# Kernel tuning notes

Measured on AMD Instinct MI355X. Metric: run time of the kernel, lower is better.

## Reference

```python
import jax, jax.numpy as jnp
import numpy as np

N = 50000          # nodes (multiple of p+e=8)
E = 400000         # edges (avg degree 8)
H, C = 4, 128      # heads, per-head channels
IN = 5             # input node feature dim
HID = 512          # mlp hidden dim
P, EV = 4, 4       # pursuers / evaders per graph
NEG_SLOPE = 0.2    # GATConv leaky_relu slope

# static team index: nodes with idx % (P+EV) < P  (team='pursuer')
_idx = np.arange(N)
TEAM_IDX = jnp.asarray(_idx[_idx % (P + EV) < P])  # [N/2]


def setup_inputs() -> dict:
    key = jax.random.key(0)
    ks = jax.random.split(key, 16)
    s = 0.1
    return {
        "x": jax.random.normal(ks[0], (N, IN), jnp.float32),
        "edge_index": jax.random.randint(ks[1], (2, E), 0, N, jnp.int64),
        "edge_attr": jax.random.normal(ks[2], (E, 2), jnp.float32),
        # GATConv params
        "W": jax.random.normal(ks[3], (H * C, IN), jnp.float32) * s,
        "att_src": jax.random.normal(ks[4], (H, C), jnp.float32) * s,
        "att_dst": jax.random.normal(ks[5], (H, C), jnp.float32) * s,
        "bias": jnp.zeros((H * C,), jnp.float32),
        # MLP head params
        "W1": jax.random.normal(ks[6], (HID, H * C), jnp.float32) * s,
        "b1": jnp.zeros((HID,), jnp.float32),
        "W2": jax.random.normal(ks[7], (HID, HID), jnp.float32) * s,
        "b2": jnp.zeros((HID,), jnp.float32),
        "W3": jax.random.normal(ks[8], (2, HID), jnp.float32) * s,
        "b3": jnp.zeros((2,), jnp.float32),
    }


def _gat_max(x, src, dst, W, att_src, att_dst, bias):
    # linear transform: [N, H, C]
    h = (x @ W.T).reshape(N, H, C)
    a_src = jnp.einsum("nhc,hc->nh", h, att_src)  # [N, H]
    a_dst = jnp.einsum("nhc,hc->nh", h, att_dst)  # [N, H]
    # per-edge attention logits, leaky relu
    alpha = jax.nn.leaky_relu(a_src[src] + a_dst[dst], NEG_SLOPE)  # [Et, H]
    # segment softmax over incoming edges of each dst node
    amax = jax.ops.segment_max(alpha, dst, num_segments=N)  # [N, H]
    ex = jnp.exp(alpha - amax[dst])
    den = jax.ops.segment_sum(ex, dst, num_segments=N)      # [N, H]
    attn = ex / den[dst]                                     # [Et, H]
    # alpha-weighted messages, scatter-MAX aggregation (aggr='max')
    msg = h[src] * attn[:, :, None]                          # [Et, H, C]
    out = jax.ops.segment_max(msg, dst, num_segments=N)     # [N, H, C]
    return out.reshape(N, H * C) + bias


def reference(x, edge_index, edge_attr, W, att_src, att_dst, bias,
              W1, b1, W2, b2, W3, b3):
    # PyG GATConv default add_self_loops=True; edge_attr ignored (edge_dim=None)
    loops = jnp.arange(N, dtype=edge_index.dtype)
    src = jnp.concatenate([edge_index[0], loops])
    dst = jnp.concatenate([edge_index[1], loops])
    emb = _gat_max(x, src, dst, W, att_src, att_dst, bias)  # [N, 512]
    h = emb[TEAM_IDX]                                        # [N/2, 512]
    h = jax.nn.relu(h @ W1.T + b1)
    h = jax.nn.relu(h @ W2.T + b2)
    return jnp.tanh(h @ W3.T + b3)                           # [N/2, 2]
```

## Files before the change

kernel.cpp:

```cpp
#include <hip/hip_runtime.h>
#include <hip/hip_bf16.h>
#include <math.h>

#define N_NODES 50000
#define N_EDGES 400000
#define HEADS   4
#define HC      512
#define IN_DIM  5
#define M_SEL   25000
#define NEG_SLOPE 0.2f

typedef __attribute__((ext_vector_type(8))) short bf16x8;
typedef __attribute__((ext_vector_type(4))) float f32x4;

__device__ inline unsigned short f2bf(float f) {
    union { float f; unsigned u; } v; v.f = f;
    unsigned r = v.u + 0x7FFF + ((v.u >> 16) & 1);
    return (unsigned short)(r >> 16);
}
__device__ inline float bf2f(unsigned short b) {
    union { unsigned u; float f; } v; v.u = ((unsigned)b) << 16;
    return v.f;
}

#define GLOAD_LDS16(g, l)                                                  \
    __builtin_amdgcn_global_load_lds(                                      \
        (const __attribute__((address_space(1))) unsigned int*)(g),        \
        (__attribute__((address_space(3))) unsigned int*)(l), 16, 0, 0)

__global__ void k_init(const float* __restrict__ W1, const float* __restrict__ W2,
                       unsigned short* __restrict__ W1b, unsigned short* __restrict__ W2b,
                       float* __restrict__ part, int* __restrict__ deg) {
    int i = blockIdx.x * 256 + threadIdx.x;
    const float* src = (i < 65536) ? W1 : W2;
    unsigned short* dst = (i < 65536) ? W1b : W2b;
    int j = i & 65535;
    float4 v = ((const float4*)src)[j];
    ushort4 o;
    o.x = f2bf(v.x); o.y = f2bf(v.y); o.z = f2bf(v.z); o.w = f2bf(v.w);
    ((ushort4*)dst)[j] = o;
    if (i < 2 * M_SEL) part[i] = 0.f;
    if (i < N_NODES) deg[i] = 1;
}

#define TR_NPW 8
#define TR_BLKS 1563

__global__ __launch_bounds__(256) void k_transform_hist(
        const float* __restrict__ x, const float* __restrict__ W,
        const float* __restrict__ att_src, const float* __restrict__ att_dst,
        unsigned short* __restrict__ h, float* __restrict__ a_src,
        float* __restrict__ a_dst, const int* __restrict__ ei,
        int* __restrict__ deg) {
    if (blockIdx.x >= TR_BLKS) {
        int e = (blockIdx.x - TR_BLKS) * 256 + threadIdx.x;
        if (e < N_EDGES) atomicAdd(&deg[ei[N_EDGES + e]], 1);
        return;
    }
    int wave = threadIdx.x >> 6, lane = threadIdx.x & 63;
    int c0 = lane * 8;

    float wreg[40];
    const float4* wp = (const float4*)(W + c0 * IN_DIM);
#pragma unroll
    for (int i = 0; i < 10; i++) ((float4*)wreg)[i] = wp[i];
    float sas[8], sad[8];
    *(float4*)&sas[0] = *(const float4*)(att_src + c0);
    *(float4*)&sas[4] = *(const float4*)(att_src + c0 + 4);
    *(float4*)&sad[0] = *(const float4*)(att_dst + c0);
    *(float4*)&sad[4] = *(const float4*)(att_dst + c0 + 4);

    int n0 = (blockIdx.x * 4 + wave) * TR_NPW;
#pragma unroll
    for (int t = 0; t < TR_NPW; t++) {
        int n = n0 + t;
        if (n >= N_NODES) return;
        float xv[IN_DIM];
#pragma unroll
        for (int i = 0; i < IN_DIM; i++) xv[i] = x[n * IN_DIM + i];

        float ps = 0.f, pd = 0.f;
        bf16x8 hv8;
#pragma unroll
        for (int j = 0; j < 8; j++) {
            float acc = 0.f;
#pragma unroll
            for (int i = 0; i < IN_DIM; i++) acc += xv[i] * wreg[j * IN_DIM + i];
            hv8[j] = (short)f2bf(acc);
            ps += acc * sas[j];
            pd += acc * sad[j];
        }
        *(bf16x8*)(h + (size_t)n * HC + c0) = hv8;

#pragma unroll
        for (int off = 8; off >= 1; off >>= 1) {
            ps += __shfl_xor(ps, off);
            pd += __shfl_xor(pd, off);
        }
        if ((lane & 15) == 0) {
            int head = lane >> 4;
            a_src[n * HEADS + head] = ps;
            a_dst[n * HEADS + head] = pd;
        }
    }
}

#define NSCAN_BLK 196

__global__ void k_scan1(const int* __restrict__ deg, int* __restrict__ excl,
                        int* __restrict__ bsum) {
    __shared__ int s[256];
    int i = blockIdx.x * 256 + threadIdx.x;
    int v = (i < N_NODES) ? deg[i] : 0;
    s[threadIdx.x] = v;
    __syncthreads();
    for (int off = 1; off < 256; off <<= 1) {
        int t = (threadIdx.x >= off) ? s[threadIdx.x - off] : 0;
        __syncthreads();
        s[threadIdx.x] += t;
        __syncthreads();
    }
    if (i < N_NODES) excl[i] = s[threadIdx.x] - v;
    if (threadIdx.x == 255) bsum[blockIdx.x] = s[255];
}

__global__ void k_scan3fill(const int* __restrict__ excl, const int* __restrict__ bsum,
                            int* __restrict__ offs, int* __restrict__ curs,
                            int* __restrict__ csr) {
    __shared__ int part[256];
    int tid = threadIdx.x;
    part[tid] = (tid < NSCAN_BLK) ? bsum[tid] : 0;
    __syncthreads();
    for (int off = 1; off < 256; off <<= 1) {
        int t = (tid >= off) ? part[tid - off] : 0;
        __syncthreads();
        part[tid] += t;
        __syncthreads();
    }
    int blockoff = (blockIdx.x == 0) ? 0 : part[blockIdx.x - 1];
    int i = blockIdx.x * 256 + tid;
    if (i < N_NODES) {
        int o = excl[i] + blockoff;
        offs[i] = o;
        csr[o] = i;
        curs[i] = o + 1;
    }
}

__global__ void k_fill_edges(const int* __restrict__ ei, int* __restrict__ cursor,
                             int* __restrict__ csr) {
    int e = blockIdx.x * 256 + threadIdx.x;
    if (e < N_EDGES) {
        int d = ei[N_EDGES + e];
        int pos = atomicAdd(&cursor[d], 1);
        csr[pos] = ei[e];
    }
}

__global__ void k_aggregate(const unsigned short* __restrict__ h, const float* __restrict__ a_src,
                            const float* __restrict__ a_dst, const int* __restrict__ csr,
                            const int* __restrict__ offs, const int* __restrict__ deg,
                            const float* __restrict__ bias, unsigned short* __restrict__ emb_sel) {
    int wave = threadIdx.x >> 6, lane = threadIdx.x & 63;
    int w = blockIdx.x * 4 + wave;
    if (w >= M_SEL) return;
    int n = ((w >> 2) << 3) + (w & 3);

    int base = offs[n];
    int dn = deg[n];
    int head = lane >> 4, egrp = lane & 15;
    int c0 = lane * 8;

    float acc[8];
#pragma unroll
    for (int j = 0; j < 8; j++) acc[j] = -INFINITY;

    if (dn <= 16) {
        int s_e = 0;
        float t = -INFINITY;
        if (egrp < dn) {
            s_e = csr[base + egrp];
            t = a_src[s_e * HEADS + head] + a_dst[n * HEADS + head];
            t = (t > 0.f) ? t : NEG_SLOPE * t;
        }
        float m = t;
#pragma unroll
        for (int off = 8; off >= 1; off >>= 1) m = fmaxf(m, __shfl_xor(m, off));
        float ex = (egrp < dn) ? __expf(t - m) : 0.f;
        float den = ex;
#pragma unroll
        for (int off = 8; off >= 1; off >>= 1) den += __shfl_xor(den, off);
        float attn = ex / den;

        int e = 0;
        for (; e + 4 <= dn; e += 4) {
            int s0 = __shfl(s_e, e + 0), s1 = __shfl(s_e, e + 1);
            int s2 = __shfl(s_e, e + 2), s3 = __shfl(s_e, e + 3);
            float a0 = __shfl(attn, (head << 4) | (e + 0));
            float a1 = __shfl(attn, (head << 4) | (e + 1));
            float a2 = __shfl(attn, (head << 4) | (e + 2));
            float a3 = __shfl(attn, (head << 4) | (e + 3));
            bf16x8 v0 = *(const bf16x8*)(h + (size_t)s0 * HC + c0);
            bf16x8 v1 = *(const bf16x8*)(h + (size_t)s1 * HC + c0);
            bf16x8 v2 = *(const bf16x8*)(h + (size_t)s2 * HC + c0);
            bf16x8 v3 = *(const bf16x8*)(h + (size_t)s3 * HC + c0);
#pragma unroll
            for (int j = 0; j < 8; j++) {
                acc[j] = fmaxf(acc[j], bf2f((unsigned short)v0[j]) * a0);
                acc[j] = fmaxf(acc[j], bf2f((unsigned short)v1[j]) * a1);
                acc[j] = fmaxf(acc[j], bf2f((unsigned short)v2[j]) * a2);
                acc[j] = fmaxf(acc[j], bf2f((unsigned short)v3[j]) * a3);
            }
        }
        for (; e < dn; e++) {
            int s = __shfl(s_e, e);
            float a = __shfl(attn, (head << 4) | e);
            bf16x8 v = *(const bf16x8*)(h + (size_t)s * HC + c0);
#pragma unroll
            for (int j = 0; j < 8; j++)
                acc[j] = fmaxf(acc[j], bf2f((unsigned short)v[j]) * a);
        }
    } else {
        float adn = a_dst[n * HEADS + head];
        float m = -INFINITY;
        for (int e0 = 0; e0 < dn; e0 += 16) {
            int e = e0 + egrp;
            if (e < dn) {
                int s = csr[base + e];
                float t = a_src[s * HEADS + head] + adn;
                t = (t > 0.f) ? t : NEG_SLOPE * t;
                m = fmaxf(m, t);
            }
        }
#pragma unroll
        for (int off = 8; off >= 1; off >>= 1) m = fmaxf(m, __shfl_xor(m, off));
        float den = 0.f;
        for (int e0 = 0; e0 < dn; e0 += 16) {
            int e = e0 + egrp;
            if (e < dn) {
                int s = csr[base + e];
                float t = a_src[s * HEADS + head] + adn;
                t = (t > 0.f) ? t : NEG_SLOPE * t;
                den += __expf(t - m);
            }
        }
#pragma unroll
        for (int off = 8; off >= 1; off >>= 1) den += __shfl_xor(den, off);
        float invden = 1.0f / den;
        for (int e = 0; e < dn; e++) {
            int s = csr[base + e];
            float t = a_src[s * HEADS + head] + adn;
            t = (t > 0.f) ? t : NEG_SLOPE * t;
            float attn = __expf(t - m) * invden;
            bf16x8 hv = *(const bf16x8*)(h + (size_t)s * HC + c0);
#pragma unroll
            for (int j = 0; j < 8; j++)
                acc[j] = fmaxf(acc[j], bf2f((unsigned short)hv[j]) * attn);
        }
    }

    bf16x8 ov;
#pragma unroll
    for (int j = 0; j < 8; j++) ov[j] = (short)f2bf(acc[j] + bias[c0 + j]);
    *(bf16x8*)(emb_sel + (size_t)w * HC + c0) = ov;
}

template <int MODE>
__global__ __launch_bounds__(256, 2) void k_gemm(const unsigned short* __restrict__ A, int M,
                                                 const unsigned short* __restrict__ Wt,
                                                 const float* __restrict__ bias,
                                                 unsigned short* __restrict__ C,
                                                 const float* __restrict__ W3,
                                                 float* __restrict__ part) {
    __shared__ unsigned short As[256 * 64];
    __shared__ unsigned short Bs[128 * 64];
    int tid = threadIdx.x;
    int m0 = blockIdx.y * 256;
    int o0 = blockIdx.x * 128;
    int wv = tid >> 6, lane = tid & 63;

    f32x4 acc[4][8];
#pragma unroll
    for (int i = 0; i < 4; i++)
#pragma unroll
        for (int j = 0; j < 8; j++) acc[i][j] = (f32x4){0.f, 0.f, 0.f, 0.f};

    for (int k0 = 0; k0 < HC; k0 += 64) {
#pragma unroll
        for (int c = 0; c < 8; c++) {
            int off = c * 4096 + tid * 16;
            int row = off >> 7, col = (off & 127) >> 1;
            GLOAD_LDS16(A + (size_t)(m0 + row) * HC + k0 + col, (char*)As + off);
        }
#pragma unroll
        for (int c = 0; c < 4; c++) {
            int off = c * 4096 + tid * 16;
            int row = off >> 7, col = (off & 127) >> 1;
            GLOAD_LDS16(Wt + (size_t)(o0 + row) * HC + k0 + col, (char*)Bs + off);
        }
        __syncthreads();

#pragma unroll
        for (int kk = 0; kk < 2; kk++) {
            int kb = kk * 32 + (lane >> 4) * 8;
            bf16x8 af[4], bfr[8];
#pragma unroll
            for (int mi = 0; mi < 4; mi++)
                af[mi] = *(const bf16x8*)(&As[(wv * 64 + mi * 16 + (lane & 15)) * 64 + kb]);
#pragma unroll
            for (int ni = 0; ni < 8; ni++)
                bfr[ni] = *(const bf16x8*)(&Bs[(ni * 16 + (lane & 15)) * 64 + kb]);
#pragma unroll
            for (int mi = 0; mi < 4; mi++)
#pragma unroll
                for (int ni = 0; ni < 8; ni++)
                    acc[mi][ni] = __builtin_amdgcn_mfma_f32_16x16x32_bf16(
                        af[mi], bfr[ni], acc[mi][ni], 0, 0, 0);
        }
        __syncthreads();
    }

    if (MODE == 0) {
#pragma unroll
        for (int ni = 0; ni < 8; ni++) {
            int ncol = o0 + ni * 16 + (lane & 15);
            float bv = bias[ncol];
#pragma unroll
            for (int mi = 0; mi < 4; mi++) {
                int mbase = m0 + wv * 64 + mi * 16 + (lane >> 4) * 4;
#pragma unroll
                for (int r = 0; r < 4; r++) {
                    int m = mbase + r;
                    if (m < M) {
                        float v = fmaxf(acc[mi][ni][r] + bv, 0.f);
                        C[(size_t)m * HC + ncol] = f2bf(v);
                    }
                }
            }
        }
    } else {
        float p0[4][4], p1[4][4];
#pragma unroll
        for (int mi = 0; mi < 4; mi++)
#pragma unroll
            for (int r = 0; r < 4; r++) { p0[mi][r] = 0.f; p1[mi][r] = 0.f; }
#pragma unroll
        for (int ni = 0; ni < 8; ni++) {
            int ncol = o0 + ni * 16 + (lane & 15);
            float bv = bias[ncol];
            float w0 = W3[ncol], w1 = W3[HC + ncol];
#pragma unroll
            for (int mi = 0; mi < 4; mi++)
#pragma unroll
                for (int r = 0; r < 4; r++) {
                    float v = fmaxf(acc[mi][ni][r] + bv, 0.f);
                    p0[mi][r] += v * w0;
                    p1[mi][r] += v * w1;
                }
        }
#pragma unroll
        for (int mi = 0; mi < 4; mi++)
#pragma unroll
            for (int r = 0; r < 4; r++) {
                float a0 = p0[mi][r], a1 = p1[mi][r];
#pragma unroll
                for (int off = 8; off >= 1; off >>= 1) {
                    a0 += __shfl_xor(a0, off);
                    a1 += __shfl_xor(a1, off);
                }
                int m = m0 + wv * 64 + mi * 16 + (lane >> 4) * 4 + r;
                if ((lane & 15) == 0 && m < M) {
                    atomicAdd(&part[m * 2 + 0], a0);
                    atomicAdd(&part[m * 2 + 1], a1);
                }
            }
    }
}

__global__ void k_tanh(const float* __restrict__ part, const float* __restrict__ b3,
                       float* __restrict__ out) {
    int i = blockIdx.x * 256 + threadIdx.x;
    if (i < 2 * M_SEL) out[i] = tanhf(part[i] + b3[i & 1]);
}

extern "C" void kernel_launch(void* const* d_in, const int* in_sizes, int n_in,
                              void* d_out, int out_size, void* d_ws, size_t ws_size,
                              hipStream_t stream) {
    const float* x       = (const float*)d_in[0];
    const int*   ei      = (const int*)d_in[1];
    const float* W       = (const float*)d_in[3];
    const float* att_src = (const float*)d_in[4];
    const float* att_dst = (const float*)d_in[5];
    const float* bias    = (const float*)d_in[6];
    const float* W1      = (const float*)d_in[7];
    const float* b1      = (const float*)d_in[8];
    const float* W2      = (const float*)d_in[9];
    const float* b2      = (const float*)d_in[10];
    const float* W3      = (const float*)d_in[11];
    const float* b3      = (const float*)d_in[12];
    float* out = (float*)d_out;

    char* ws = (char*)d_ws;
    unsigned short* h       = (unsigned short*)(ws);
    unsigned short* emb_sel = (unsigned short*)(ws + 51200000);
    unsigned short* h1      = (unsigned short*)(ws + 76800000);
    float* part  = (float*)(ws + 102400000);
    float* a_src = (float*)(ws + 102600000);
    float* a_dst = (float*)(ws + 103400000);
    int*   deg   = (int*)  (ws + 104200000);
    int*   offs  = (int*)  (ws + 104400000);
    int*   curs  = (int*)  (ws + 104600000);
    int*   excl  = (int*)  (ws + 104800000);
    int*   bsum  = (int*)  (ws + 105000000);
    int*   csr   = (int*)  (ws + 105001024);
    unsigned short* W1b = (unsigned short*)(ws + 106801024);
    unsigned short* W2b = (unsigned short*)(ws + 107325312);

    k_init<<<512, 256, 0, stream>>>(W1, W2, W1b, W2b, part, deg);
    k_transform_hist<<<TR_BLKS * 2, 256, 0, stream>>>(x, W, att_src, att_dst, h,
                                                      a_src, a_dst, ei, deg);
    k_scan1<<<NSCAN_BLK, 256, 0, stream>>>(deg, excl, bsum);
    k_scan3fill<<<NSCAN_BLK, 256, 0, stream>>>(excl, bsum, offs, curs, csr);
    k_fill_edges<<<(N_EDGES + 255) / 256, 256, 0, stream>>>(ei, curs, csr);
    k_aggregate<<<6250, 256, 0, stream>>>(h, a_src, a_dst, csr, offs, deg, bias, emb_sel);

    dim3 g(4, 98);
    k_gemm<0><<<g, 256, 0, stream>>>(emb_sel, M_SEL, W1b, b1, h1, nullptr, nullptr);
    k_gemm<1><<<g, 256, 0, stream>>>(h1, M_SEL, W2b, b2, nullptr, W3, part);
    k_tanh<<<196, 256, 0, stream>>>(part, b3, out);
}
```

Before: 178.2 us.

## Fuse tanh epilogue into second GEMM via last-block counter and XCD-aware block mapping

```diff
diff --git a/kernel.cpp b/kernel.cpp
--- a/kernel.cpp
+++ b/kernel.cpp
@@ -30,7 +30,8 @@
 
 __global__ void k_init(const float* __restrict__ W1, const float* __restrict__ W2,
                        unsigned short* __restrict__ W1b, unsigned short* __restrict__ W2b,
-                       float* __restrict__ part, int* __restrict__ deg) {
+                       float* __restrict__ part, int* __restrict__ deg,
+                       int* __restrict__ done) {
     int i = blockIdx.x * 256 + threadIdx.x;
     const float* src = (i < 65536) ? W1 : W2;
     unsigned short* dst = (i < 65536) ? W1b : W2b;
@@ -41,6 +42,7 @@
     ((ushort4*)dst)[j] = o;
     if (i < 2 * M_SEL) part[i] = 0.f;
     if (i < N_NODES) deg[i] = 1;
+    if (i < 128) done[i] = 0;
 }
 
 #define TR_NPW 8
@@ -271,12 +273,20 @@
                                                  const float* __restrict__ bias,
                                                  unsigned short* __restrict__ C,
                                                  const float* __restrict__ W3,
-                                                 float* __restrict__ part) {
+                                                 float* __restrict__ part,
+                                                 int* __restrict__ done,
+                                                 const float* __restrict__ b3,
+                                                 float* __restrict__ outp) {
     __shared__ unsigned short As[256 * 64];
     __shared__ unsigned short Bs[128 * 64];
     int tid = threadIdx.x;
-    int m0 = blockIdx.y * 256;
-    int o0 = blockIdx.x * 128;
+    int bid = blockIdx.x;
+    int xcd = bid & 7, q = bid >> 3;
+    int p = xcd + 8 * (q >> 2);
+    int xb = q & 3;
+    if (p >= 98) return;
+    int m0 = p * 256;
+    int o0 = xb * 128;
     int wv = tid >> 6, lane = tid & 63;
 
     f32x4 acc[4][8];
@@ -374,13 +384,26 @@
                     atomicAdd(&part[m * 2 + 1], a1);
                 }
             }
-    }
-}
-
-__global__ void k_tanh(const float* __restrict__ part, const float* __restrict__ b3,
-                       float* __restrict__ out) {
-    int i = blockIdx.x * 256 + threadIdx.x;
-    if (i < 2 * M_SEL) out[i] = tanhf(part[i] + b3[i & 1]);
+
+        __syncthreads();
+        __shared__ int lastf;
+        if (tid == 0) {
+            __threadfence();
+            int old = atomicAdd(&done[p], 1);
+            lastf = (old == 3);
+        }
+        __syncthreads();
+        if (lastf) {
+            for (int i = tid; i < 512; i += 256) {
+                int idx = p * 512 + i;
+                if (idx < 2 * M_SEL) {
+                    float v = __hip_atomic_load(&part[idx], __ATOMIC_RELAXED,
+                                                __HIP_MEMORY_SCOPE_AGENT);
+                    outp[idx] = tanhf(v + b3[i & 1]);
+                }
+            }
+        }
+    }
 }
 
 extern "C" void kernel_launch(void* const* d_in, const int* in_sizes, int n_in,
@@ -412,11 +435,12 @@
     int*   curs  = (int*)  (ws + 104600000);
     int*   excl  = (int*)  (ws + 104800000);
     int*   bsum  = (int*)  (ws + 105000000);
-    int*   csr   = (int*)  (ws + 105001024);
-    unsigned short* W1b = (unsigned short*)(ws + 106801024);
-    unsigned short* W2b = (unsigned short*)(ws + 107325312);
-
-    k_init<<<512, 256, 0, stream>>>(W1, W2, W1b, W2b, part, deg);
+    int*   done  = (int*)  (ws + 105001024);
+    int*   csr   = (int*)  (ws + 105001536);
+    unsigned short* W1b = (unsigned short*)(ws + 106801536);
+    unsigned short* W2b = (unsigned short*)(ws + 107325824);
+
+    k_init<<<512, 256, 0, stream>>>(W1, W2, W1b, W2b, part, deg, done);
     k_transform_hist<<<TR_BLKS * 2, 256, 0, stream>>>(x, W, att_src, att_dst, h,
                                                       a_src, a_dst, ei, deg);
     k_scan1<<<NSCAN_BLK, 256, 0, stream>>>(deg, excl, bsum);
@@ -424,8 +448,8 @@
     k_fill_edges<<<(N_EDGES + 255) / 256, 256, 0, stream>>>(ei, curs, csr);
     k_aggregate<<<6250, 256, 0, stream>>>(h, a_src, a_dst, csr, offs, deg, bias, emb_sel);
 
-    dim3 g(4, 98);
-    k_gemm<0><<<g, 256, 0, stream>>>(emb_sel, M_SEL, W1b, b1, h1, nullptr, nullptr);
-    k_gemm<1><<<g, 256, 0, stream>>>(h1, M_SEL, W2b, b2, nullptr, W3, part);
-    k_tanh<<<196, 256, 0, stream>>>(part, b3, out);
-}
+    k_gemm<0><<<416, 256, 0, stream>>>(emb_sel, M_SEL, W1b, b1, h1, nullptr, nullptr,
+                                       nullptr, nullptr, nullptr);
+    k_gemm<1><<<416, 256, 0, stream>>>(h1, M_SEL, W2b, b2, nullptr, W3, part,
+                                       done, b3, out);
+}
```

Result: faster. 174.4 us (median of 2 runs) (-2.2%).
